# Kernel tuning notes

Measured on AMD Instinct MI355X. Metric: run time of the kernel, lower is better.

Reference implementation:

```python
import jax, jax.numpy as jnp
import numpy as np

E = 1_600_000          # number of edge messages
D = 128                # feature dim (hard-coded in module)
P = 2                  # var_num_patches
PD = D // P            # var_effective_patch_dim = 64
N_NODES = 50_000       # dim_size


def setup_inputs() -> dict:
    key = jax.random.key(0)
    k1, k2, k3 = jax.random.split(key, 3)
    x = jax.random.normal(k1, (E, D), dtype=jnp.float32)
    index = jax.random.randint(k2, (E,), 0, N_NODES, dtype=jnp.int64)
    # Linear(64 -> 128, bias=False): torch weight layout [out, in] = [128, 64]
    W = jax.random.normal(k3, (D, PD), dtype=jnp.float32) * 0.05
    learnable_param = jnp.zeros((1,), dtype=jnp.float32) + 1e-05
    return {"x": x, "W": W, "learnable_param": learnable_param,
            "index": index, "dim": 0, "dim_size": N_NODES}


def reference(x, W, learnable_param, index, dim, dim_size):
    e = x.reshape(-1, D)                       # [E, 128]
    e1 = e.reshape(-1, P, PD)                  # [E, 2, 64]
    # fc_all then clamp(0,1): [E, 2, 128]
    gates = jnp.clip(jnp.einsum('npd,od->npo', e1, W), 0.0, 1.0)
    # split gate output into P chunks of PD along last axis: [E, 2(patch), 2(chunk), 64]
    g = gates.reshape(-1, P, P, PD)
    # for each chunk c: sum over patch p of e1[:,p,:] * g[:,p,c,:]  -> [E, 2, 64]
    out = jnp.einsum('npd,npcd->ncd', e1, g).reshape(-1, D)   # [E, 128]
    # dual scatter-sum over destination nodes
    out_original = jax.ops.segment_sum(e, index, num_segments=dim_size)   # [N, 128]
    out_s = jax.ops.segment_sum(out, index, num_segments=dim_size)       # [N, 128]
    return jnp.abs(learnable_param) * out_s + out_original
```

## Files before the change

kernel.cpp:

```cpp
#include <hip/hip_runtime.h>


#define D  128
#define PD 64

__global__ __launch_bounds__(256, 4) void agg_gated_scatter_kernel(
    const float* __restrict__ x,
    const float* __restrict__ W,
    const float* __restrict__ lp_ptr,
    const int*  __restrict__ index,
    float* __restrict__ out,
    int E, int nIter)
{
    const int tid = threadIdx.x;
    const int g   = tid >> 7;
    const int o   = tid & 127;
    const int d0  = o & 63;

    __shared__ float sh_e[2][D];

    float w[PD];
    const float4* Wrow = reinterpret_cast<const float4*>(W + o * PD);
    #pragma unroll
    for (int i = 0; i < PD / 4; ++i) {
        float4 t = Wrow[i];
        w[4*i+0] = t.x; w[4*i+1] = t.y; w[4*i+2] = t.z; w[4*i+3] = t.w;
    }

    const float lp = fabsf(lp_ptr[0]);

    const long long groupCount = (long long)gridDim.x * 2;
    long long edge = (long long)blockIdx.x * 2 + g;

    for (int it = 0; it < nIter; ++it) {
        const bool active = (edge < (long long)E);
        float e_val = 0.0f;
        int   idx   = 0;
        if (active) {
            e_val = x[edge * D + o];
            idx   = index[edge];
            sh_e[g][o] = e_val;
        }
        __syncthreads();

        if (active) {
            const float4* sh4 = reinterpret_cast<const float4*>(&sh_e[g][0]);
            float acc0 = 0.0f, acc1 = 0.0f;
            #pragma unroll
            for (int i = 0; i < 16; ++i) {
                float4 ea = sh4[i];
                float4 eb = sh4[16 + i];
                acc0 = fmaf(ea.x, w[4*i+0], acc0);
                acc0 = fmaf(ea.y, w[4*i+1], acc0);
                acc0 = fmaf(ea.z, w[4*i+2], acc0);
                acc0 = fmaf(ea.w, w[4*i+3], acc0);
                acc1 = fmaf(eb.x, w[4*i+0], acc1);
                acc1 = fmaf(eb.y, w[4*i+1], acc1);
                acc1 = fmaf(eb.z, w[4*i+2], acc1);
                acc1 = fmaf(eb.w, w[4*i+3], acc1);
            }
            const float g0 = fminf(fmaxf(acc0, 0.0f), 1.0f);
            const float g1 = fminf(fmaxf(acc1, 0.0f), 1.0f);

            const float ep0 = sh_e[g][d0];
            const float ep1 = sh_e[g][64 + d0];
            const float v   = e_val + lp * (ep0 * g0 + ep1 * g1);

            atomicAdd(out + (long long)idx * D + o, v);
        }
        __syncthreads();
        edge += groupCount;
    }
}

extern "C" void kernel_launch(void* const* d_in, const int* in_sizes, int n_in,
                              void* d_out, int out_size, void* d_ws, size_t ws_size,
                              hipStream_t stream) {
    const float* x     = (const float*)d_in[0];
    const float* W     = (const float*)d_in[1];
    const float* lp    = (const float*)d_in[2];
    const int*   index = (const int*)d_in[3];
    float*       out   = (float*)d_out;

    const int E = in_sizes[0] / D;

    hipMemsetAsync(d_out, 0, (size_t)out_size * sizeof(float), stream);

    const int block = 256;
    const int grid  = 2048;
    const long long groups = (long long)grid * 2;
    const int nIter = (int)(((long long)E + groups - 1) / groups);

    agg_gated_scatter_kernel<<<grid, block, 0, stream>>>(x, W, lp, index, out, E, nIter);
}
```

Before: 1.886 ms.

## Compute gate projection with bf16 MFMA over per-wave 16-edge tiles

Replaces the per-thread scalar FMA gate computation with bf16 MFMA 16x16x32 instructions, each wave processing a 16-edge tile staged in padded shared memory. Block-wide barriers are removed because each wave owns its own shared buffers and index slots. W is converted to bf16 fragments held in registers. This trades gate precision (bf16 inputs) for far less ALU work, and relies on in-wave LDS ordering without explicit barriers.

```diff
diff --git a/kernel.cpp b/kernel.cpp
--- a/kernel.cpp
+++ b/kernel.cpp
@@ -1,75 +1,144 @@
 #include <hip/hip_runtime.h>
 
 
-#define D  128
-#define PD 64
+#define D   128
+#define PD  64
+#define EPW 16
+#define RS  132
 
-__global__ __launch_bounds__(256, 4) void agg_gated_scatter_kernel(
+typedef float  f32x4  __attribute__((ext_vector_type(4)));
+typedef __bf16 bf16x8 __attribute__((ext_vector_type(8)));
+
+static __device__ __forceinline__ float clamp01(float v) {
+    return fminf(fmaxf(v, 0.0f), 1.0f);
+}
+
+__global__ __launch_bounds__(256, 3) void agg_mfma_kernel(
     const float* __restrict__ x,
     const float* __restrict__ W,
     const float* __restrict__ lp_ptr,
     const int*  __restrict__ index,
     float* __restrict__ out,
-    int E, int nIter)
+    int E, int nTiles)
 {
-    const int tid = threadIdx.x;
-    const int g   = tid >> 7;
-    const int o   = tid & 127;
-    const int d0  = o & 63;
+    const int tid  = threadIdx.x;
+    const int wave = tid >> 6;
+    const int lane = tid & 63;
+    const int q    = lane >> 4;
+    const int c    = lane & 15;
 
-    __shared__ float sh_e[2][D];
+    __shared__ float shx_all[4][EPW * RS];
+    __shared__ int   shidx_all[4][EPW];
+    float* shx   = shx_all[wave];
+    int*   shidx = shidx_all[wave];
 
-    float w[PD];
-    const float4* Wrow = reinterpret_cast<const float4*>(W + o * PD);
+    bf16x8 bfrag[8][2];
     #pragma unroll
-    for (int i = 0; i < PD / 4; ++i) {
-        float4 t = Wrow[i];
-        w[4*i+0] = t.x; w[4*i+1] = t.y; w[4*i+2] = t.z; w[4*i+3] = t.w;
+    for (int nt = 0; nt < 8; ++nt) {
+        #pragma unroll
+        for (int ks = 0; ks < 2; ++ks) {
+            const float* wp = W + (nt * 16 + c) * PD + ks * 32 + q * 8;
+            f32x4 w0 = *(const f32x4*)(wp);
+            f32x4 w1 = *(const f32x4*)(wp + 4);
+            bf16x8 f;
+            f[0] = (__bf16)w0[0]; f[1] = (__bf16)w0[1];
+            f[2] = (__bf16)w0[2]; f[3] = (__bf16)w0[3];
+            f[4] = (__bf16)w1[0]; f[5] = (__bf16)w1[1];
+            f[6] = (__bf16)w1[2]; f[7] = (__bf16)w1[3];
+            bfrag[nt][ks] = f;
+        }
     }
 
     const float lp = fabsf(lp_ptr[0]);
 
-    const long long groupCount = (long long)gridDim.x * 2;
-    long long edge = (long long)blockIdx.x * 2 + g;
+    const int waveStride = gridDim.x * 4;
+    for (int t = blockIdx.x * 4 + wave; t < nTiles; t += waveStride) {
+        const long long e0 = (long long)t * EPW;
+        const int remEdges = (int)((E - e0) < EPW ? (E - e0) : EPW);
+        const int validV4  = remEdges * 32;
 
-    for (int it = 0; it < nIter; ++it) {
-        const bool active = (edge < (long long)E);
-        float e_val = 0.0f;
-        int   idx   = 0;
-        if (active) {
-            e_val = x[edge * D + o];
-            idx   = index[edge];
-            sh_e[g][o] = e_val;
+        const float4* xg = (const float4*)(x + e0 * D);
+        #pragma unroll
+        for (int i = 0; i < 8; ++i) {
+            const int v4 = lane + i * 64;
+            float4 val = make_float4(0.f, 0.f, 0.f, 0.f);
+            if (v4 < validV4) val = xg[v4];
+            const int g4   = v4 * 4;
+            const int edge = g4 >> 7;
+            const int col  = g4 & 127;
+            *(float4*)&shx[edge * RS + col] = val;
         }
-        __syncthreads();
+        if (lane < EPW)
+            shidx[lane] = (lane < remEdges) ? index[e0 + lane] : 0;
 
-        if (active) {
-            const float4* sh4 = reinterpret_cast<const float4*>(&sh_e[g][0]);
-            float acc0 = 0.0f, acc1 = 0.0f;
+        #pragma unroll
+        for (int mt = 0; mt < 2; ++mt) {
+            const int rowl = mt * 16 + c;
+            const int el   = rowl >> 1;
+            const int p    = rowl & 1;
+            bf16x8 afrag[2];
             #pragma unroll
-            for (int i = 0; i < 16; ++i) {
-                float4 ea = sh4[i];
-                float4 eb = sh4[16 + i];
-                acc0 = fmaf(ea.x, w[4*i+0], acc0);
-                acc0 = fmaf(ea.y, w[4*i+1], acc0);
-                acc0 = fmaf(ea.z, w[4*i+2], acc0);
-                acc0 = fmaf(ea.w, w[4*i+3], acc0);
-                acc1 = fmaf(eb.x, w[4*i+0], acc1);
-                acc1 = fmaf(eb.y, w[4*i+1], acc1);
-                acc1 = fmaf(eb.z, w[4*i+2], acc1);
-                acc1 = fmaf(eb.w, w[4*i+3], acc1);
+            for (int ks = 0; ks < 2; ++ks) {
+                const float* ap = &shx[el * RS + p * PD + ks * 32 + q * 8];
+                f32x4 a0 = *(const f32x4*)(ap);
+                f32x4 a1 = *(const f32x4*)(ap + 4);
+                bf16x8 f;
+                f[0] = (__bf16)a0[0]; f[1] = (__bf16)a0[1];
+                f[2] = (__bf16)a0[2]; f[3] = (__bf16)a0[3];
+                f[4] = (__bf16)a1[0]; f[5] = (__bf16)a1[1];
+                f[6] = (__bf16)a1[2]; f[7] = (__bf16)a1[3];
+                afrag[ks] = f;
             }
-            const float g0 = fminf(fmaxf(acc0, 0.0f), 1.0f);
-            const float g1 = fminf(fmaxf(acc1, 0.0f), 1.0f);
 
-            const float ep0 = sh_e[g][d0];
-            const float ep1 = sh_e[g][64 + d0];
-            const float v   = e_val + lp * (ep0 * g0 + ep1 * g1);
+            f32x4 acc[8];
+            #pragma unroll
+            for (int nt = 0; nt < 8; ++nt) {
+                acc[nt] = (f32x4){0.f, 0.f, 0.f, 0.f};
+                acc[nt] = __builtin_amdgcn_mfma_f32_16x16x32_bf16(
+                              afrag[0], bfrag[nt][0], acc[nt], 0, 0, 0);
+                acc[nt] = __builtin_amdgcn_mfma_f32_16x16x32_bf16(
+                              afrag[1], bfrag[nt][1], acc[nt], 0, 0, 0);
+            }
 
-            atomicAdd(out + (long long)idx * D + o, v);
+            const int  eAl   = mt * 8 + q * 2;
+            const int  eBl   = eAl + 1;
+            const int  nodeA = shidx[eAl];
+            const int  nodeB = shidx[eBl];
+            const bool okA   = (e0 + eAl) < E;
+            const bool okB   = (e0 + eBl) < E;
+            float* outA = out + (long long)nodeA * D + c;
+            float* outB = out + (long long)nodeB * D + c;
+
+            #pragma unroll
+            for (int dg = 0; dg < 4; ++dg) {
+                const int d = dg * 16 + c;
+                const float aA0 = shx[eAl * RS + d];
+                const float aA1 = shx[eAl * RS + 64 + d];
+                const float aB0 = shx[eBl * RS + d];
+                const float aB1 = shx[eBl * RS + 64 + d];
+
+                const f32x4 g0 = acc[dg];
+                const f32x4 g1 = acc[dg + 4];
+                const float gA0 = clamp01(g0[0]), gA1 = clamp01(g0[1]);
+                const float gB0 = clamp01(g0[2]), gB1 = clamp01(g0[3]);
+                const float hA0 = clamp01(g1[0]), hA1 = clamp01(g1[1]);
+                const float hB0 = clamp01(g1[2]), hB1 = clamp01(g1[3]);
+
+                const float vA0 = aA0 + lp * (aA0 * gA0 + aA1 * gA1);
+                const float vA1 = aA1 + lp * (aA0 * hA0 + aA1 * hA1);
+                const float vB0 = aB0 + lp * (aB0 * gB0 + aB1 * gB1);
+                const float vB1 = aB1 + lp * (aB0 * hB0 + aB1 * hB1);
+
+                if (okA) {
+                    atomicAdd(outA + dg * 16,      vA0);
+                    atomicAdd(outA + 64 + dg * 16, vA1);
+                }
+                if (okB) {
+                    atomicAdd(outB + dg * 16,      vB0);
+                    atomicAdd(outB + 64 + dg * 16, vB1);
+                }
+            }
         }
-        __syncthreads();
-        edge += groupCount;
     }
 }
 
@@ -82,14 +151,12 @@
     const int*   index = (const int*)d_in[3];
     float*       out   = (float*)d_out;
 
-    const int E = in_sizes[0] / D;
+    const int E      = in_sizes[0] / D;
+    const int nTiles = (E + EPW - 1) / EPW;
 
     hipMemsetAsync(d_out, 0, (size_t)out_size * sizeof(float), stream);
 
-    const int block = 256;
-    const int grid  = 2048;
-    const long long groups = (long long)grid * 2;
-    const int nIter = (int)(((long long)E + groups - 1) / groups);
-
-    agg_gated_scatter_kernel<<<grid, block, 0, stream>>>(x, W, lp, index, out, E, nIter);
+    int grid = (nTiles + 3) / 4;
+    if (grid > 2560) grid = 2560;
+    agg_mfma_kernel<<<grid, 256, 0, stream>>>(x, W, lp, index, out, E, nTiles);
 }
```

After: 1.516 ms. 1.24x faster.
